# Kernel optimization log

Measured on AMD Instinct MI355X. Metric: run time of the kernel, lower is better.

## Reference

```python
import jax, jax.numpy as jnp
import numpy as np
from jax import lax

N, H, W, T = 8, 100, 152, 256
STRIDE = 8
ANCHOR_SIZE = 64.0
PRE_NMS_THRESH = 0.05
PRE_NMS_TOP_N = 1000
NMS_THRESH = 0.6
POST_TOP_N = 100
IMG_H, IMG_W = 800, 1216
BW = (10.0, 10.0, 5.0, 5.0)          # BoxCoder weights (wx, wy, ww, wh)
DWH_CLIP = float(np.log(1000.0 / 16.0))
TO_REMOVE = 1.0


def setup_inputs() -> dict:
    key = jax.random.key(0)
    k1, k2, k3 = jax.random.split(key, 3)
    box_regression = jax.random.normal(k1, (N, 4, H, W), dtype=jnp.float32)
    centerness = jax.random.normal(k2, (N, 1, H, W), dtype=jnp.float32)
    dot_product_logits = jax.random.normal(k3, (N, H * W, T), dtype=jnp.float32)
    # anchor grid matching permute_and_flatten's (H, W, A) row-major ordering
    ys, xs = jnp.meshgrid(jnp.arange(H, dtype=jnp.float32),
                          jnp.arange(W, dtype=jnp.float32), indexing="ij")
    cx = xs.reshape(-1) * STRIDE + STRIDE / 2.0
    cy = ys.reshape(-1) * STRIDE + STRIDE / 2.0
    half = ANCHOR_SIZE / 2.0
    anc = jnp.stack([cx - half, cy - half, cx + half, cy + half], axis=-1)  # [H*W, 4]
    anchors = jnp.broadcast_to(anc, (N, H * W, 4)).astype(jnp.float32)
    return {"box_regression": box_regression, "centerness": centerness,
            "anchors": anchors, "dot_product_logits": dot_product_logits}


def _decode(rel, anc):
    w = anc[..., 2] - anc[..., 0] + TO_REMOVE
    h = anc[..., 3] - anc[..., 1] + TO_REMOVE
    cx = anc[..., 0] + 0.5 * w
    cy = anc[..., 1] + 0.5 * h
    dx = rel[..., 0] / BW[0]
    dy = rel[..., 1] / BW[1]
    dw = jnp.minimum(rel[..., 2] / BW[2], DWH_CLIP)
    dh = jnp.minimum(rel[..., 3] / BW[3], DWH_CLIP)
    pcx = dx * w + cx
    pcy = dy * h + cy
    pw = jnp.exp(dw) * w
    ph = jnp.exp(dh) * h
    return jnp.stack([pcx - 0.5 * pw, pcy - 0.5 * ph,
                      pcx + 0.5 * pw - 1.0, pcy + 0.5 * ph - 1.0], axis=-1)


def _iou_one_vs_all(box, boxes):
    area1 = (box[2] - box[0] + TO_REMOVE) * (box[3] - box[1] + TO_REMOVE)
    area2 = (boxes[:, 2] - boxes[:, 0] + TO_REMOVE) * (boxes[:, 3] - boxes[:, 1] + TO_REMOVE)
    lt = jnp.maximum(box[:2], boxes[:, :2])
    rb = jnp.minimum(box[2:], boxes[:, 2:])
    wh = jnp.maximum(rb - lt + TO_REMOVE, 0.0)
    inter = wh[:, 0] * wh[:, 1]
    return inter / (area1 + area2 - inter)


def _nms_single(boxes, scores):
    # greedy NMS, fixed POST_TOP_N iterations (fpn_post_nms_top_n)
    def step(s, _):
        j = jnp.argmax(s)
        sj = s[j]
        bj = boxes[j]
        flag = (sj > 0).astype(boxes.dtype)
        ious = _iou_one_vs_all(bj, boxes)
        s = jnp.where(ious > NMS_THRESH, 0.0, s).at[j].set(0.0)
        return s, (bj * flag, sj * flag)
    _, (kb, ks) = lax.scan(step, scores, None, length=POST_TOP_N)
    return kb, ks


def reference(box_regression, centerness, anchors, dot_product_logits):
    n, _, h, w = box_regression.shape
    # sigmoid + MEAN token aggregation  -> [N, HWA]
    scores = jax.nn.sigmoid(dot_product_logits).mean(-1)
    # permute_and_flatten: [N,4A,H,W] -> [N, HWA, 4]
    box_reg = box_regression.reshape(n, 1, 4, h, w).transpose(0, 3, 4, 1, 2).reshape(n, -1, 4)
    ctr = jax.nn.sigmoid(centerness.reshape(n, 1, 1, h, w).transpose(0, 3, 4, 1, 2).reshape(n, -1))
    cand = scores > PRE_NMS_THRESH          # threshold on raw aggregated scores
    cls = scores * ctr                      # centerness-weighted score
    masked = jnp.where(cand, cls, 0.0)
    vals, idx = lax.top_k(masked, PRE_NMS_TOP_N)          # per-image top-k candidates
    valid = jnp.take_along_axis(cand, idx, axis=1)        # [N, PRE_NMS_TOP_N]
    sel_reg = jnp.take_along_axis(box_reg, idx[..., None], axis=1)
    sel_anc = jnp.take_along_axis(anchors, idx[..., None], axis=1)
    boxes = _decode(sel_reg, sel_anc)
    # clip_to_image
    boxes = jnp.stack([
        jnp.clip(boxes[..., 0], 0.0, IMG_W - 1.0),
        jnp.clip(boxes[..., 1], 0.0, IMG_H - 1.0),
        jnp.clip(boxes[..., 2], 0.0, IMG_W - 1.0),
        jnp.clip(boxes[..., 3], 0.0, IMG_H - 1.0)], axis=-1)
    vf = valid.astype(boxes.dtype)
    det_scores = jnp.sqrt(jnp.where(valid, vals, 1.0)) * vf   # sqrt of cls*ctr, safe grad
    keep_boxes, keep_scores = jax.vmap(_nms_single)(boxes, det_scores)
    return keep_boxes, keep_scores
```

## Files before the change

kernel.cpp:

```cpp
#include <hip/hip_runtime.h>
#include <math.h>

#define NN 8
#define HH 100
#define WW 152
#define HW (HH*WW)
#define TT 256
#define TOPN 1000
#define POSTN 100
#define NMS_T 0.6f
#define IMGW 1216
#define IMGH 800
#define DWH_CLIP 4.135166556742356f

typedef unsigned long long u64;
typedef unsigned int u32;

__global__ __launch_bounds__(256) void score_kernel(
    const float* __restrict__ logits,
    const float* __restrict__ centerness,
    float* __restrict__ masked)
{
    int wid  = blockIdx.x * 4 + (threadIdx.x >> 6);
    int lane = threadIdx.x & 63;
    const float4 v = *(reinterpret_cast<const float4*>(logits + (size_t)wid * TT) + lane);
    float s = 0.f;
    s += __fdividef(1.f, 1.f + expf(-v.x));
    s += __fdividef(1.f, 1.f + expf(-v.y));
    s += __fdividef(1.f, 1.f + expf(-v.z));
    s += __fdividef(1.f, 1.f + expf(-v.w));
    #pragma unroll
    for (int off = 32; off; off >>= 1) s += __shfl_xor(s, off, 64);
    if (lane == 0) {
        float score = s * (1.0f / 256.0f);
        float c = centerness[wid];
        float ctr = 1.f / (1.f + expf(-c));
        masked[wid] = (score > 0.05f) ? score * ctr : 0.f;
    }
}

__global__ __launch_bounds__(256) void select_nms_kernel(
    const float* __restrict__ masked,
    const float* __restrict__ box_reg,
    float* __restrict__ out)
{
    const int n   = blockIdx.x;
    const int tid = threadIdx.x;
    const int wv  = tid >> 6;
    const int PER = (HW + 255) / 256;

    u32 bits[PER];
    const float* mb = masked + (size_t)n * HW;
    #pragma unroll
    for (int j = 0; j < PER; j++) {
        int e = tid + j * 256;
        bits[j] = (e < HW) ? __float_as_uint(mb[e]) : 0u;
    }

    __shared__ int   parts[2][4];
    __shared__ u64   keys[256];
    __shared__ float4 sbox[256];
    __shared__ float  sscr[256];
    __shared__ int   s_cnt1, s_cnt2;
    __shared__ int   s_state;

    float* outb = out + (size_t)n * POSTN * 4;
    float* outs = out + (size_t)NN * POSTN * 4 + (size_t)n * POSTN;

    float ax1 = 0.f, ay1 = 0.f, ax2 = 0.f, ay2 = 0.f;
    float bx1 = 0.f, by1 = 0.f, bx2 = 0.f, by2 = 0.f;
    int   kept = 0;
    bool  done = false;

    u32 thrPrev = 0xFFFFFFFFu;
    int  p = 0;

    for (int b = 0; b < 4 && !done; ++b) {
        const int target = 256 * (b + 1) - 1;
        u32 lo = 0u;
        u32 hi = (thrPrev < 0x3F800000u) ? thrPrev : 0x3F800000u;
        while (lo < hi) {
            u32 mid = lo + ((hi - lo) >> 1);
            int c = 0;
            #pragma unroll
            for (int j = 0; j < PER; j++) c += (bits[j] > mid) ? 1 : 0;
            #pragma unroll
            for (int off = 32; off; off >>= 1) c += __shfl_xor(c, off, 64);
            if ((tid & 63) == 0) parts[p][wv] = c;
            __syncthreads();
            int tot = parts[p][0] + parts[p][1] + parts[p][2] + parts[p][3];
            p ^= 1;
            if (tot <= target) hi = mid; else lo = mid + 1;
        }
        const u32 thr = lo;

        if (tid == 0) { s_cnt1 = 0; s_cnt2 = 0; }
        keys[tid] = 0ull;
        __syncthreads();
        #pragma unroll
        for (int j = 0; j < PER; j++) {
            int e = tid + j * 256;
            u32 v = bits[j];
            if (e < HW && v > thr && v < thrPrev) {
                int pos = atomicAdd(&s_cnt1, 1);
                if (pos < 256) keys[pos] = (((u64)v) << 32) | (u32)(~e);
            }
        }
        __syncthreads();
        const int c1 = min(s_cnt1, 256);
        #pragma unroll
        for (int j = 0; j < PER; j++) {
            int e = tid + j * 256;
            if (e < HW && bits[j] == thr) {
                int q = atomicAdd(&s_cnt2, 1);
                if (c1 + q < 256) keys[c1 + q] = (((u64)thr) << 32) | (u32)(~e);
            }
        }
        __syncthreads();

        for (int k = 2; k <= 256; k <<= 1) {
            for (int j2 = k >> 1; j2 > 0; j2 >>= 1) {
                int ixj = tid ^ j2;
                if (ixj > tid) {
                    u64 a = keys[tid], bb = keys[ixj];
                    bool sw = ((tid & k) == 0) ? (a < bb) : (a > bb);
                    if (sw) { keys[tid] = bb; keys[ixj] = a; }
                }
                __syncthreads();
            }
        }

        {
            u64 kk = keys[tid];
            float s = __uint_as_float((u32)(kk >> 32));
            float4 box = make_float4(0.f, 0.f, 0.f, 0.f);
            float scr = 0.f;
            if (s > 0.f) {
                int loc = (int)(~(u32)kk);
                float acx = (float)(loc % WW) * 8.f + 4.f;
                float acy = (float)(loc / WW) * 8.f + 4.f;
                float a0 = acx - 32.f, a1 = acy - 32.f, a2 = acx + 32.f, a3 = acy + 32.f;
                float r0 = box_reg[((size_t)n * 4 + 0) * HW + loc];
                float r1 = box_reg[((size_t)n * 4 + 1) * HW + loc];
                float r2 = box_reg[((size_t)n * 4 + 2) * HW + loc];
                float r3 = box_reg[((size_t)n * 4 + 3) * HW + loc];
                float w  = a2 - a0 + 1.0f;
                float h  = a3 - a1 + 1.0f;
                float cx = a0 + 0.5f * w;
                float cy = a1 + 0.5f * h;
                float dx = r0 / 10.0f;
                float dy = r1 / 10.0f;
                float dw = fminf(r2 / 5.0f, DWH_CLIP);
                float dh = fminf(r3 / 5.0f, DWH_CLIP);
                float pcx = dx * w + cx;
                float pcy = dy * h + cy;
                float pw  = expf(dw) * w;
                float ph  = expf(dh) * h;
                float x1 = pcx - 0.5f * pw;
                float y1 = pcy - 0.5f * ph;
                float x2 = pcx + 0.5f * pw - 1.0f;
                float y2 = pcy + 0.5f * ph - 1.0f;
                box.x = fminf(fmaxf(x1, 0.f), (float)(IMGW - 1));
                box.y = fminf(fmaxf(y1, 0.f), (float)(IMGH - 1));
                box.z = fminf(fmaxf(x2, 0.f), (float)(IMGW - 1));
                box.w = fminf(fmaxf(y2, 0.f), (float)(IMGH - 1));
                scr = sqrtf(s);
            }
            sbox[tid] = box;
            sscr[tid] = scr;
        }
        __syncthreads();

        if (tid < 64) {
            const int limit = (b == 3) ? (TOPN - 3 * 256) : 256;
            for (int i = 0; i < limit; ++i) {
                float s = sscr[i];
                if (s <= 0.f) { done = true; break; }
                float4 cb = sbox[i];
                float carea = (cb.z - cb.x + 1.f) * (cb.w - cb.y + 1.f);

                float ix1 = fmaxf(cb.x, ax1), iy1 = fmaxf(cb.y, ay1);
                float ix2 = fminf(cb.z, ax2), iy2 = fminf(cb.w, ay2);
                float iw = fmaxf(ix2 - ix1 + 1.f, 0.f), ih = fmaxf(iy2 - iy1 + 1.f, 0.f);
                float interA = iw * ih;
                float areaA = (ax2 - ax1 + 1.f) * (ay2 - ay1 + 1.f);
                float iouA = interA / (carea + areaA - interA);

                ix1 = fmaxf(cb.x, bx1); iy1 = fmaxf(cb.y, by1);
                ix2 = fminf(cb.z, bx2); iy2 = fminf(cb.w, by2);
                iw = fmaxf(ix2 - ix1 + 1.f, 0.f); ih = fmaxf(iy2 - iy1 + 1.f, 0.f);
                float interB = iw * ih;
                float areaB = (bx2 - bx1 + 1.f) * (by2 - by1 + 1.f);
                float iouB = interB / (carea + areaB - interB);

                bool supA = (tid < kept)      && (iouA > NMS_T);
                bool supB = (tid < kept - 64) && (iouB > NMS_T);
                u64 sup = __ballot(supA) | __ballot(supB);
                if (sup == 0ull) {
                    if (kept < 64) {
                        if (tid == kept)      { ax1 = cb.x; ay1 = cb.y; ax2 = cb.z; ay2 = cb.w; }
                    } else {
                        if (tid == kept - 64) { bx1 = cb.x; by1 = cb.y; bx2 = cb.z; by2 = cb.w; }
                    }
                    if (tid == 0) {
                        outb[kept * 4 + 0] = cb.x; outb[kept * 4 + 1] = cb.y;
                        outb[kept * 4 + 2] = cb.z; outb[kept * 4 + 3] = cb.w;
                        outs[kept] = s;
                    }
                    ++kept;
                    if (kept == POSTN) { done = true; break; }
                }
            }
            if (tid == 0) s_state = kept | (done ? 0x10000 : 0);
        }
        __syncthreads();
        done = (s_state >> 16) != 0;
        thrPrev = thr;
    }

    const int cnt = s_state & 0xFFFF;
    for (int i = cnt + tid; i < POSTN; i += 256) {
        outb[i * 4 + 0] = 0.f; outb[i * 4 + 1] = 0.f;
        outb[i * 4 + 2] = 0.f; outb[i * 4 + 3] = 0.f;
        outs[i] = 0.f;
    }
}

extern "C" void kernel_launch(void* const* d_in, const int* in_sizes, int n_in,
                              void* d_out, int out_size, void* d_ws, size_t ws_size,
                              hipStream_t stream) {
    const float* box_reg = (const float*)d_in[0];
    const float* center  = (const float*)d_in[1];
    const float* logits  = (const float*)d_in[3];
    float* out = (float*)d_out;

    float* masked = (float*)d_ws;

    score_kernel<<<(NN * HW) / 4, 256, 0, stream>>>(logits, center, masked);
    select_nms_kernel<<<NN, 256, 0, stream>>>(masked, box_reg, out);
}
```

Baseline: 260.1 us.

## Replace serial per-candidate NMS with parallel IoU bitmask and ballot-based greedy scan

Instead of one wavefront walking candidates one at a time and checking each against the kept boxes, all 256 threads now build a 256x256 IoU suppression bitmask in shared memory and test each candidate against previously kept boxes. A single wavefront then runs greedy selection over the bitmask using ballots and ffs, stepping only over surviving candidates. This targets the latency-bound serial NMS loop, at the cost of a full O(256^2) IoU computation per batch and extra shared memory, which may lower occupancy.

Result: slower. 273.5 us (+5.2%).

```diff
diff --git a/kernel.cpp b/kernel.cpp
--- a/kernel.cpp
+++ b/kernel.cpp
@@ -57,25 +57,28 @@
         bits[j] = (e < HW) ? __float_as_uint(mb[e]) : 0u;
     }
 
-    __shared__ int   parts[2][4];
-    __shared__ u64   keys[256];
+    __shared__ int    parts[2][4];
+    __shared__ u64    keys[256];
     __shared__ float4 sbox[256];
     __shared__ float  sscr[256];
-    __shared__ int   s_cnt1, s_cnt2;
-    __shared__ int   s_state;
+    __shared__ float  sarea[256];
+    __shared__ u64    smask[256 * 4];
+    __shared__ unsigned char ssupp[256];
+    __shared__ float4 kbox[POSTN + 4];
+    __shared__ int    keep_list[POSTN + 4];
+    __shared__ int    s_cnt1, s_cnt2, s_nvalid, s_newkept;
 
     float* outb = out + (size_t)n * POSTN * 4;
     float* outs = out + (size_t)NN * POSTN * 4 + (size_t)n * POSTN;
 
-    float ax1 = 0.f, ay1 = 0.f, ax2 = 0.f, ay2 = 0.f;
-    float bx1 = 0.f, by1 = 0.f, bx2 = 0.f, by2 = 0.f;
-    int   kept = 0;
-    bool  done = false;
-
-    u32 thrPrev = 0xFFFFFFFFu;
+    int  kept_total = 0;
+    bool done = false;
+    u32  thrPrev = 0xFFFFFFFFu;
     int  p = 0;
 
     for (int b = 0; b < 4 && !done; ++b) {
+        const int limit = (b == 3) ? (TOPN - 3 * 256) : 256;
+
         const int target = 256 * (b + 1) - 1;
         u32 lo = 0u;
         u32 hi = (thrPrev < 0x3F800000u) ? thrPrev : 0x3F800000u;
@@ -94,8 +97,9 @@
         }
         const u32 thr = lo;
 
-        if (tid == 0) { s_cnt1 = 0; s_cnt2 = 0; }
+        if (tid == 0) { s_cnt1 = 0; s_cnt2 = 0; s_nvalid = 0; s_newkept = 0; }
         keys[tid] = 0ull;
+        ssupp[tid] = 0;
         __syncthreads();
         #pragma unroll
         for (int j = 0; j < PER; j++) {
@@ -130,11 +134,11 @@
             }
         }
 
+        float4 myb = make_float4(0.f, 0.f, 0.f, 0.f);
+        float   myscr = 0.f;
         {
             u64 kk = keys[tid];
             float s = __uint_as_float((u32)(kk >> 32));
-            float4 box = make_float4(0.f, 0.f, 0.f, 0.f);
-            float scr = 0.f;
             if (s > 0.f) {
                 int loc = (int)(~(u32)kk);
                 float acx = (float)(loc % WW) * 8.f + 4.f;
@@ -160,66 +164,109 @@
                 float y1 = pcy - 0.5f * ph;
                 float x2 = pcx + 0.5f * pw - 1.0f;
                 float y2 = pcy + 0.5f * ph - 1.0f;
-                box.x = fminf(fmaxf(x1, 0.f), (float)(IMGW - 1));
-                box.y = fminf(fmaxf(y1, 0.f), (float)(IMGH - 1));
-                box.z = fminf(fmaxf(x2, 0.f), (float)(IMGW - 1));
-                box.w = fminf(fmaxf(y2, 0.f), (float)(IMGH - 1));
-                scr = sqrtf(s);
-            }
-            sbox[tid] = box;
-            sscr[tid] = scr;
+                myb.x = fminf(fmaxf(x1, 0.f), (float)(IMGW - 1));
+                myb.y = fminf(fmaxf(y1, 0.f), (float)(IMGH - 1));
+                myb.z = fminf(fmaxf(x2, 0.f), (float)(IMGW - 1));
+                myb.w = fminf(fmaxf(y2, 0.f), (float)(IMGH - 1));
+                myscr = sqrtf(s);
+                if (tid < limit) atomicAdd(&s_nvalid, 1);
+            }
+            sbox[tid] = myb;
+            sscr[tid] = myscr;
+            sarea[tid] = (myb.z - myb.x + 1.f) * (myb.w - myb.y + 1.f);
+        }
+        __syncthreads();
+
+        if (kept_total > 0 && myscr > 0.f) {
+            float marea = sarea[tid];
+            for (int k = 0; k < kept_total; ++k) {
+                float4 kb = kbox[k];
+                float ix1 = fmaxf(myb.x, kb.x), iy1 = fmaxf(myb.y, kb.y);
+                float ix2 = fminf(myb.z, kb.z), iy2 = fminf(myb.w, kb.w);
+                float iw = fmaxf(ix2 - ix1 + 1.f, 0.f), ih = fmaxf(iy2 - iy1 + 1.f, 0.f);
+                float inter = iw * ih;
+                float karea = (kb.z - kb.x + 1.f) * (kb.w - kb.y + 1.f);
+                float iou = inter / (marea + karea - inter);
+                if (iou > NMS_T) { ssupp[tid] = 1; break; }
+            }
+        }
+
+        {
+            u64 m0 = 0, m1 = 0, m2 = 0, m3 = 0;
+            if (myscr > 0.f) {
+                float marea = sarea[tid];
+                for (int j = 0; j < 256; ++j) {
+                    float4 ob = sbox[j];
+                    float ix1 = fmaxf(myb.x, ob.x), iy1 = fmaxf(myb.y, ob.y);
+                    float ix2 = fminf(myb.z, ob.z), iy2 = fminf(myb.w, ob.w);
+                    float iw = fmaxf(ix2 - ix1 + 1.f, 0.f), ih = fmaxf(iy2 - iy1 + 1.f, 0.f);
+                    float inter = iw * ih;
+                    float iou = inter / (marea + sarea[j] - inter);
+                    if (iou > NMS_T) {
+                        u64 bit = 1ull << (j & 63);
+                        switch (j >> 6) {
+                            case 0: m0 |= bit; break;
+                            case 1: m1 |= bit; break;
+                            case 2: m2 |= bit; break;
+                            default: m3 |= bit; break;
+                        }
+                    }
+                }
+            }
+            smask[tid * 4 + 0] = m0;
+            smask[tid * 4 + 1] = m1;
+            smask[tid * 4 + 2] = m2;
+            smask[tid * 4 + 3] = m3;
         }
         __syncthreads();
 
         if (tid < 64) {
-            const int limit = (b == 3) ? (TOPN - 3 * 256) : 256;
-            for (int i = 0; i < limit; ++i) {
-                float s = sscr[i];
-                if (s <= 0.f) { done = true; break; }
-                float4 cb = sbox[i];
-                float carea = (cb.z - cb.x + 1.f) * (cb.w - cb.y + 1.f);
-
-                float ix1 = fmaxf(cb.x, ax1), iy1 = fmaxf(cb.y, ay1);
-                float ix2 = fminf(cb.z, ax2), iy2 = fminf(cb.w, ay2);
-                float iw = fmaxf(ix2 - ix1 + 1.f, 0.f), ih = fmaxf(iy2 - iy1 + 1.f, 0.f);
-                float interA = iw * ih;
-                float areaA = (ax2 - ax1 + 1.f) * (ay2 - ay1 + 1.f);
-                float iouA = interA / (carea + areaA - interA);
-
-                ix1 = fmaxf(cb.x, bx1); iy1 = fmaxf(cb.y, by1);
-                ix2 = fminf(cb.z, bx2); iy2 = fminf(cb.w, by2);
-                iw = fmaxf(ix2 - ix1 + 1.f, 0.f); ih = fmaxf(iy2 - iy1 + 1.f, 0.f);
-                float interB = iw * ih;
-                float areaB = (bx2 - bx1 + 1.f) * (by2 - by1 + 1.f);
-                float iouB = interB / (carea + areaB - interB);
-
-                bool supA = (tid < kept)      && (iouA > NMS_T);
-                bool supB = (tid < kept - 64) && (iouB > NMS_T);
-                u64 sup = __ballot(supA) | __ballot(supB);
-                if (sup == 0ull) {
-                    if (kept < 64) {
-                        if (tid == kept)      { ax1 = cb.x; ay1 = cb.y; ax2 = cb.z; ay2 = cb.w; }
-                    } else {
-                        if (tid == kept - 64) { bx1 = cb.x; by1 = cb.y; bx2 = cb.z; by2 = cb.w; }
-                    }
-                    if (tid == 0) {
-                        outb[kept * 4 + 0] = cb.x; outb[kept * 4 + 1] = cb.y;
-                        outb[kept * 4 + 2] = cb.z; outb[kept * 4 + 3] = cb.w;
-                        outs[kept] = s;
-                    }
-                    ++kept;
-                    if (kept == POSTN) { done = true; break; }
-                }
-            }
-            if (tid == 0) s_state = kept | (done ? 0x10000 : 0);
-        }
-        __syncthreads();
-        done = (s_state >> 16) != 0;
+            const int l = tid;
+            u32 alive = 0;
+            #pragma unroll
+            for (int k = 0; k < 4; k++) {
+                int i = 4 * l + k;
+                if (i < limit && sscr[i] > 0.f && ssupp[i] == 0) alive |= (1u << k);
+            }
+            int newkept = 0;
+            while (kept_total + newkept < POSTN) {
+                u64 bal = __ballot(alive != 0u);
+                if (bal == 0ull) break;
+                int w = __ffsll(bal) - 1;
+                u32 aw = __shfl(alive, w, 64);
+                int c = __ffs(aw) - 1;
+                int i = 4 * w + c;
+                u64 row = smask[i * 4 + (l >> 4)];
+                u32 bits4 = (u32)((row >> ((4 * l) & 63)) & 0xFull);
+                alive &= ~bits4;
+                if (l == w) alive &= ~(1u << c);
+                if (l == 0) keep_list[newkept] = i;
+                ++newkept;
+            }
+            if (tid == 0) s_newkept = newkept;
+        }
+        __syncthreads();
+
+        const int nk = s_newkept;
+        if (tid < nk) {
+            int i = keep_list[tid];
+            float4 kb = sbox[i];
+            int pos = kept_total + tid;
+            outb[pos * 4 + 0] = kb.x; outb[pos * 4 + 1] = kb.y;
+            outb[pos * 4 + 2] = kb.z; outb[pos * 4 + 3] = kb.w;
+            outs[pos] = sscr[i];
+            kbox[pos] = kb;
+        }
+        __syncthreads();
+
+        const int nvalid = s_nvalid;
+        kept_total += nk;
+        done = (kept_total >= POSTN) || (nvalid < limit);
         thrPrev = thr;
-    }
-
-    const int cnt = s_state & 0xFFFF;
-    for (int i = cnt + tid; i < POSTN; i += 256) {
+        __syncthreads();
+    }
+
+    for (int i = kept_total + tid; i < POSTN; i += 256) {
         outb[i * 4 + 0] = 0.f; outb[i * 4 + 1] = 0.f;
         outb[i * 4 + 2] = 0.f; outb[i * 4 + 3] = 0.f;
         outs[i] = 0.f;
```
